# Kernel optimization log

Hardware: AMD Instinct MI355X
Metric: run time of the kernel (lower is better)

Reference implementation:

```python
import jax, jax.numpy as jnp
import numpy as np

B, T, E, H, V = 64, 21, 512, 512, 10000


def _lstm_step(x, h, c, W_ih, W_hh, b):
    # PyTorch LSTMCell gate order: i, f, g, o
    gates = x @ W_ih.T + h @ W_hh.T + b  # [B, 4H]
    i, f, g, o = jnp.split(gates, 4, axis=-1)
    i, f, o = jax.nn.sigmoid(i), jax.nn.sigmoid(f), jax.nn.sigmoid(o)
    g = jnp.tanh(g)
    c_new = f * c + i * g
    h_new = o * jnp.tanh(c_new)
    return h_new, c_new


def setup_inputs() -> dict:
    key = jax.random.key(0)
    ks = jax.random.split(key, 8)
    s_ih = 1.0 / np.sqrt(H)
    return {
        "features": jax.random.normal(ks[0], (B, E), jnp.float32),
        "caption_embedding": jax.random.normal(ks[1], (B, T, E), jnp.float32),
        "W_ih": jax.random.uniform(ks[2], (4 * H, E), jnp.float32, -s_ih, s_ih),
        "W_hh": jax.random.uniform(ks[3], (4 * H, H), jnp.float32, -s_ih, s_ih),
        "b_ih": jax.random.uniform(ks[4], (4 * H,), jnp.float32, -s_ih, s_ih),
        "b_hh": jax.random.uniform(ks[5], (4 * H,), jnp.float32, -s_ih, s_ih),
        "W_lin": jax.random.uniform(ks[6], (V, H), jnp.float32, -s_ih, s_ih),
        "b_lin": jax.random.uniform(ks[7], (V,), jnp.float32, -s_ih, s_ih),
    }


def reference(features, caption_embedding, W_ih, W_hh, b_ih, b_hh, W_lin, b_lin):
    b = b_ih + b_hh
    batch = features.shape[0]
    hidden = W_hh.shape[1]
    h0 = jnp.zeros((batch, hidden), features.dtype)
    c0 = jnp.zeros((batch, hidden), features.dtype)
    # t = 0: consume image features, no output emitted
    h, c = _lstm_step(features, h0, c0, W_ih, W_hh, b)
    # t = 1..T-1: consume caption_embedding[:, t-1], emit linear(h)
    emb_seq = jnp.swapaxes(caption_embedding[:, :-1, :], 0, 1)  # [T-1, B, E]

    def body(carry, x_t):
        h, c = carry
        h, c = _lstm_step(x_t, h, c, W_ih, W_hh, b)
        out = h @ W_lin.T + b_lin  # [B, V]
        return (h, c), out

    _, outs = jax.lax.scan(body, (h, c), emb_seq)  # [T-1, B, V]
    return jnp.swapaxes(outs, 0, 1)  # [B, T-1, V]
```

## Files before the change

### kernel.cpp

```cpp
#include <hip/hip_runtime.h>
#include <hip/hip_bf16.h>


#define NB 64
#define NT 21
#define NE 512
#define NH 512
#define NV 10000
#define G4 2048

typedef __attribute__((ext_vector_type(8))) short bf16x8;
typedef __attribute__((ext_vector_type(4))) float f32x4;
typedef __attribute__((ext_vector_type(4))) unsigned short u16x4;

#define OFF_WIH_HI   0UL
#define OFF_WIH_LO   2097152UL
#define OFF_WHH_HI   4194304UL
#define OFF_WHH_LO   6291456UL
#define OFF_WLIN_HI  8388608UL
#define OFF_XSEQ_HI  18743296UL
#define OFF_XSEQ_LO  20185088UL
#define OFF_BIAS     21626880UL
#define OFF_XIH      21635072UL
#define OFF_GHH      32645120UL
#define OFF_GHL      32776192UL
#define OFF_C        32907264UL
#define OFF_HBUF     33038336UL
#define OFF_FLG      34349056UL

__device__ inline unsigned short f2bf(float f) {
    unsigned int u = __float_as_uint(f);
    unsigned int r = u + 0x7FFFu + ((u >> 16) & 1u);
    return (unsigned short)(r >> 16);
}
__device__ inline float bf2f(unsigned short s) {
    return __uint_as_float(((unsigned int)s) << 16);
}

__device__ __forceinline__ void gl_lds16(const unsigned short* g, unsigned short* l) {
    auto gp = (const __attribute__((address_space(1))) unsigned int*)(unsigned long long)(const void*)g;
    auto lp = (__attribute__((address_space(3))) unsigned int*)(unsigned int)(unsigned long long)(void*)l;
    __builtin_amdgcn_global_load_lds(gp, lp, 16, 0, 0);
}

__device__ __forceinline__ void gl_lds16_sc(const unsigned short* g, unsigned short* l) {
    auto gp = (const __attribute__((address_space(1))) unsigned int*)(unsigned long long)(const void*)g;
    auto lp = (__attribute__((address_space(3))) unsigned int*)(unsigned int)(unsigned long long)(void*)l;
    __builtin_amdgcn_global_load_lds(gp, lp, 16, 0, 17);
}

__device__ __forceinline__ void st2_sc(unsigned short* p, unsigned short v) {
    unsigned int vv = v;
    asm volatile("global_store_short %0, %1, off sc0 sc1" :: "v"(p), "v"(vv) : "memory");
}

__global__ __launch_bounds__(256) void prep_kernel(
    const float* __restrict__ features, const float* __restrict__ cap,
    const float* __restrict__ W_ih, const float* __restrict__ W_hh,
    const float* __restrict__ b_ih, const float* __restrict__ b_hh,
    const float* __restrict__ W_lin, unsigned char* __restrict__ ws)
{
    const int idx = blockIdx.x * 256 + threadIdx.x;
    unsigned short* wih_hi = (unsigned short*)(ws + OFF_WIH_HI);
    unsigned short* wih_lo = (unsigned short*)(ws + OFF_WIH_LO);
    unsigned short* whh_hi = (unsigned short*)(ws + OFF_WHH_HI);
    unsigned short* whh_lo = (unsigned short*)(ws + OFF_WHH_LO);
    unsigned short* wlin_hi = (unsigned short*)(ws + OFF_WLIN_HI);
    unsigned short* xs_hi = (unsigned short*)(ws + OFF_XSEQ_HI);
    unsigned short* xs_lo = (unsigned short*)(ws + OFF_XSEQ_LO);
    float* bias = (float*)(ws + OFF_BIAS);

    if (idx < 262144) {
        const int i4 = idx * 4;
        float4 w = *(const float4*)(W_ih + i4);
        u16x4 hi, lo;
        hi.x = f2bf(w.x); lo.x = f2bf(w.x - bf2f(hi.x));
        hi.y = f2bf(w.y); lo.y = f2bf(w.y - bf2f(hi.y));
        hi.z = f2bf(w.z); lo.z = f2bf(w.z - bf2f(hi.z));
        hi.w = f2bf(w.w); lo.w = f2bf(w.w - bf2f(hi.w));
        *(u16x4*)(wih_hi + i4) = hi;
        *(u16x4*)(wih_lo + i4) = lo;
    } else if (idx < 524288) {
        const int i4 = (idx - 262144) * 4;
        float4 w = *(const float4*)(W_hh + i4);
        u16x4 hi, lo;
        hi.x = f2bf(w.x); lo.x = f2bf(w.x - bf2f(hi.x));
        hi.y = f2bf(w.y); lo.y = f2bf(w.y - bf2f(hi.y));
        hi.z = f2bf(w.z); lo.z = f2bf(w.z - bf2f(hi.z));
        hi.w = f2bf(w.w); lo.w = f2bf(w.w - bf2f(hi.w));
        *(u16x4*)(whh_hi + i4) = hi;
        *(u16x4*)(whh_lo + i4) = lo;
    } else if (idx < 1804288) {
        const int i4 = (idx - 524288) * 4;
        float4 w = *(const float4*)(W_lin + i4);
        u16x4 hi;
        hi.x = f2bf(w.x); hi.y = f2bf(w.y); hi.z = f2bf(w.z); hi.w = f2bf(w.w);
        *(u16x4*)(wlin_hi + i4) = hi;
    } else if (idx < 1976320) {
        const int i4 = (idx - 1804288) * 4;
        const int e = i4 & 511;
        const int b = (i4 >> 9) & 63;
        const int t = i4 >> 15;
        float4 x = (t == 0) ? *(const float4*)(features + b * NE + e)
                            : *(const float4*)(cap + b * (NT * NE) + (t - 1) * NE + e);
        u16x4 hi, lo;
        hi.x = f2bf(x.x); lo.x = f2bf(x.x - bf2f(hi.x));
        hi.y = f2bf(x.y); lo.y = f2bf(x.y - bf2f(hi.y));
        hi.z = f2bf(x.z); lo.z = f2bf(x.z - bf2f(hi.z));
        hi.w = f2bf(x.w); lo.w = f2bf(x.w - bf2f(hi.w));
        *(u16x4*)(xs_hi + i4) = hi;
        *(u16x4*)(xs_lo + i4) = lo;
    } else if (idx < 1976832) {
        const int j = (idx - 1976320) * 4;
        float4 a = *(const float4*)(b_ih + j);
        float4 b = *(const float4*)(b_hh + j);
        *(float4*)(bias + j) = make_float4(a.x + b.x, a.y + b.y, a.z + b.z, a.w + b.w);
    }
}

__global__ __launch_bounds__(256) void gemm_a_kernel(unsigned char* __restrict__ ws)
{
    __shared__ unsigned short Ah[2][4096], Al[2][4096], Bh[2][4096], Bl[2][4096];
    const int tid = threadIdx.x;
    const int lane = tid & 63, wv = tid >> 6;
    const int mf = lane & 15, kg = lane >> 4;
    const int mw = (wv >> 1) * 64, nw = (wv & 1) * 64;
    const int m0 = blockIdx.y * 128, n0 = blockIdx.x * 128;

    const unsigned short* __restrict__ xh = (const unsigned short*)(ws + OFF_XSEQ_HI);
    const unsigned short* __restrict__ xl = (const unsigned short*)(ws + OFF_XSEQ_LO);
    const unsigned short* __restrict__ wh = (const unsigned short*)(ws + OFF_WIH_HI);
    const unsigned short* __restrict__ wl = (const unsigned short*)(ws + OFF_WIH_LO);
    const float* __restrict__ bias = (const float*)(ws + OFF_BIAS);
    float* __restrict__ xih = (float*)(ws + OFF_XIH);

    f32x4 acc[4][4];
#pragma unroll
    for (int i = 0; i < 4; i++)
#pragma unroll
        for (int j = 0; j < 4; j++) acc[i][j] = (f32x4){0.f, 0.f, 0.f, 0.f};

    auto stage = [&](int buf, int k0) {
#pragma unroll
        for (int h = 0; h < 2; ++h) {
            int s = h * 256 + tid;
            int r = s >> 2, ks = (s & 3) * 8;
            gl_lds16(xh + (size_t)(m0 + r) * 512 + k0 + ks, &Ah[buf][s * 8]);
            gl_lds16(xl + (size_t)(m0 + r) * 512 + k0 + ks, &Al[buf][s * 8]);
            gl_lds16(wh + (size_t)(n0 + r) * 512 + k0 + ks, &Bh[buf][s * 8]);
            gl_lds16(wl + (size_t)(n0 + r) * 512 + k0 + ks, &Bl[buf][s * 8]);
        }
    };

    stage(0, 0);
    for (int kt = 0; kt < 16; ++kt) {
        __syncthreads();
        const int cur = kt & 1;
        if (kt < 15) stage(cur ^ 1, (kt + 1) * 32);
        bf16x8 ah[4], al[4], bh[4], bl[4];
#pragma unroll
        for (int i = 0; i < 4; i++) {
            ah[i] = *(const bf16x8*)&Ah[cur][(mw + i * 16 + mf) * 32 + kg * 8];
            al[i] = *(const bf16x8*)&Al[cur][(mw + i * 16 + mf) * 32 + kg * 8];
            bh[i] = *(const bf16x8*)&Bh[cur][(nw + i * 16 + mf) * 32 + kg * 8];
            bl[i] = *(const bf16x8*)&Bl[cur][(nw + i * 16 + mf) * 32 + kg * 8];
        }
#pragma unroll
        for (int i = 0; i < 4; i++)
#pragma unroll
            for (int j = 0; j < 4; j++) {
                acc[i][j] = __builtin_amdgcn_mfma_f32_16x16x32_bf16(ah[i], bh[j], acc[i][j], 0, 0, 0);
                acc[i][j] = __builtin_amdgcn_mfma_f32_16x16x32_bf16(ah[i], bl[j], acc[i][j], 0, 0, 0);
                acc[i][j] = __builtin_amdgcn_mfma_f32_16x16x32_bf16(al[i], bh[j], acc[i][j], 0, 0, 0);
            }
    }
#pragma unroll
    for (int i = 0; i < 4; i++)
#pragma unroll
        for (int j = 0; j < 4; j++) {
            const int col = n0 + nw + j * 16 + mf;
            const float bb = bias[col];
#pragma unroll
            for (int r = 0; r < 4; r++) {
                const int R = m0 + mw + i * 16 + kg * 4 + r;
                if (R < NT * NB) xih[(size_t)R * G4 + col] = acc[i][j][r] + bb;
            }
        }
}

__global__ __launch_bounds__(512, 2) void lstm_persistent(unsigned char* __restrict__ ws)
{
    __shared__ unsigned short Hhi[64 * 512];
    __shared__ unsigned short Hlo[64 * 512];
    __shared__ float glf[4096];
    const int tid = threadIdx.x;
    const int lane = tid & 63, wv = tid >> 6;
    const int mf = lane & 15, kg = lane >> 4;
    const int q = wv & 3;
    const int mh = wv >> 2;
    const int bc = blockIdx.x;

    unsigned short* __restrict__ ghh = (unsigned short*)(ws + OFF_GHH);
    unsigned short* __restrict__ ghl = (unsigned short*)(ws + OFF_GHL);
    const unsigned short* __restrict__ whh_hi = (const unsigned short*)(ws + OFF_WHH_HI);
    const unsigned short* __restrict__ whh_lo = (const unsigned short*)(ws + OFF_WHH_LO);
    const float* __restrict__ xih_base = (const float*)(ws + OFF_XIH);
    unsigned short* __restrict__ hbuf = (unsigned short*)(ws + OFF_HBUF);
    unsigned int* __restrict__ ctr = (unsigned int*)(ws + OFF_FLG);

    bf16x8 bh[16], blo[16];
#pragma unroll
    for (int j = 0; j < 16; ++j) {
        const size_t off = (size_t)(q * 512 + bc * 16 + mf) * 512 + j * 32 + kg * 8;
        bh[j] = *(const bf16x8*)(whh_hi + off);
        blo[j] = *(const bf16x8*)(whh_lo + off);
    }

    const int row0 = tid >> 4;
    const int row1 = row0 + 32;
    const int ci = tid & 15;
    const int c = bc * 16 + ci;
    const int jc = c >> 3;
    float creg[2] = {0.f, 0.f};

    float xp[8];
    auto load_xp = [&](int tt) {
        const float* __restrict__ xq = xih_base + (size_t)tt * NB * G4;
#pragma unroll
        for (int g = 0; g < 4; ++g) {
            xp[g]     = xq[row0 * G4 + g * 512 + c];
            xp[4 + g] = xq[row1 * G4 + g * 512 + c];
        }
    };
    load_xp(0);

    for (int t = 0; t < NT; ++t) {
        f32x4 acc[2];
        acc[0] = (f32x4){0.f, 0.f, 0.f, 0.f};
        acc[1] = (f32x4){0.f, 0.f, 0.f, 0.f};

        if (t > 0) {
            const int rd = (t + 1) & 1;
            const unsigned short* __restrict__ ghh_r = ghh + rd * (NB * NH);
            const unsigned short* __restrict__ ghl_r = ghl + rd * (NB * NH);
#pragma unroll
            for (int i = 0; i < 8; ++i) {
                const int s = i * 512 + tid;
                gl_lds16_sc(ghh_r + s * 8, &Hhi[s * 8]);
            }
#pragma unroll
            for (int i = 0; i < 8; ++i) {
                const int s = i * 512 + tid;
                gl_lds16_sc(ghl_r + s * 8, &Hlo[s * 8]);
            }
            asm volatile("s_waitcnt vmcnt(8)" ::: "memory");
            __builtin_amdgcn_s_barrier();
#pragma unroll
            for (int kt = 0; kt < 16; ++kt) {
                const int j = kt * 4 + kg;
#pragma unroll
                for (int m = 0; m < 2; ++m) {
                    const int row = mh * 32 + m * 16 + mf;
                    bf16x8 a_hi = *(const bf16x8*)&Hhi[(row * 64 + (j ^ (row & 7))) * 8];
                    acc[m] = __builtin_amdgcn_mfma_f32_16x16x32_bf16(a_hi, bh[kt], acc[m], 0, 0, 0);
                    acc[m] = __builtin_amdgcn_mfma_f32_16x16x32_bf16(a_hi, blo[kt], acc[m], 0, 0, 0);
                }
            }
            asm volatile("s_waitcnt vmcnt(0)" ::: "memory");
            __builtin_amdgcn_s_barrier();
#pragma unroll
            for (int kt = 0; kt < 16; ++kt) {
                const int j = kt * 4 + kg;
#pragma unroll
                for (int m = 0; m < 2; ++m) {
                    const int row = mh * 32 + m * 16 + mf;
                    bf16x8 a_lo = *(const bf16x8*)&Hlo[(row * 64 + (j ^ (row & 7))) * 8];
                    acc[m] = __builtin_amdgcn_mfma_f32_16x16x32_bf16(a_lo, bh[kt], acc[m], 0, 0, 0);
                }
            }
        }

#pragma unroll
        for (int m = 0; m < 2; ++m) {
            const int row = mh * 32 + m * 16 + kg * 4;
#pragma unroll
            for (int r = 0; r < 4; ++r)
                glf[(q * 64 + row + r) * 16 + mf] = acc[m][r];
        }
        __syncthreads();

        unsigned short* __restrict__ ghh_w = ghh + (t & 1) * (NB * NH);
        unsigned short* __restrict__ ghl_w = ghl + (t & 1) * (NB * NH);
#pragma unroll
        for (int cc = 0; cc < 2; ++cc) {
            const int row = cc ? row1 : row0;
            const float gi = glf[(0 * 64 + row) * 16 + ci] + xp[cc * 4 + 0];
            const float gf = glf[(1 * 64 + row) * 16 + ci] + xp[cc * 4 + 1];
            const float gg = glf[(2 * 64 + row) * 16 + ci] + xp[cc * 4 + 2];
            const float go = glf[(3 * 64 + row) * 16 + ci] + xp[cc * 4 + 3];
            const float i_ = 1.f / (1.f + __expf(-gi));
            const float f_ = 1.f / (1.f + __expf(-gf));
            const float g_ = tanhf(gg);
            const float o_ = 1.f / (1.f + __expf(-go));
            const float c_new = f_ * creg[cc] + i_ * g_;
            creg[cc] = c_new;
            const float h_new = o_ * tanhf(c_new);
            const unsigned short hi = f2bf(h_new);
            const unsigned short lo = f2bf(h_new - bf2f(hi));
            const int sw = row * 512 + ((jc ^ (row & 7)) << 3) + (c & 7);
            st2_sc(&ghh_w[sw], hi);
            st2_sc(&ghl_w[sw], lo);
            if (t >= 1)
                __builtin_nontemporal_store(hi, &hbuf[(t - 1) * (NB * NH) + row * NH + c]);
        }

        if (t < NT - 1) {
            load_xp(t + 1);
            asm volatile("s_waitcnt vmcnt(0)" ::: "memory");
            __syncthreads();
            if (tid == 0) {
                __hip_atomic_fetch_add(&ctr[t], 1u, __ATOMIC_RELAXED, __HIP_MEMORY_SCOPE_AGENT);
                while (__hip_atomic_load(&ctr[t], __ATOMIC_RELAXED, __HIP_MEMORY_SCOPE_AGENT) < 32u)
                    __builtin_amdgcn_s_sleep(1);
            }
            __syncthreads();
        }
    }
}

__global__ __launch_bounds__(256) void gemm_c_kernel(
    unsigned char* __restrict__ ws, const float* __restrict__ b_lin, float* __restrict__ out)
{
    __shared__ unsigned short As[2][4096], Bs[2][4096];
    const int tid = threadIdx.x;
    const int lane = tid & 63, wv = tid >> 6;
    const int mf = lane & 15, kg = lane >> 4;
    const int mw = (wv >> 1) * 64, nw = (wv & 1) * 64;
    const int m0 = blockIdx.y * 128, n0 = blockIdx.x * 128;

    const unsigned short* __restrict__ hb = (const unsigned short*)(ws + OFF_HBUF);
    const unsigned short* __restrict__ wlin = (const unsigned short*)(ws + OFF_WLIN_HI);

    f32x4 acc[4][4];
#pragma unroll
    for (int i = 0; i < 4; i++)
#pragma unroll
        for (int j = 0; j < 4; j++) acc[i][j] = (f32x4){0.f, 0.f, 0.f, 0.f};

    auto stage = [&](int buf, int k0) {
#pragma unroll
        for (int h = 0; h < 2; ++h) {
            int s = h * 256 + tid;
            int r = s >> 2, ks = (s & 3) * 8;
            gl_lds16(hb + (size_t)(m0 + r) * 512 + k0 + ks, &As[buf][s * 8]);
            gl_lds16(wlin + (size_t)(n0 + r) * 512 + k0 + ks, &Bs[buf][s * 8]);
        }
    };

    stage(0, 0);
    for (int kt = 0; kt < 16; ++kt) {
        __syncthreads();
        const int cur = kt & 1;
        if (kt < 15) stage(cur ^ 1, (kt + 1) * 32);
        bf16x8 af[4], bf[4];
#pragma unroll
        for (int i = 0; i < 4; i++) {
            af[i] = *(const bf16x8*)&As[cur][(mw + i * 16 + mf) * 32 + kg * 8];
            bf[i] = *(const bf16x8*)&Bs[cur][(nw + i * 16 + mf) * 32 + kg * 8];
        }
#pragma unroll
        for (int i = 0; i < 4; i++)
#pragma unroll
            for (int j = 0; j < 4; j++)
                acc[i][j] = __builtin_amdgcn_mfma_f32_16x16x32_bf16(af[i], bf[j], acc[i][j], 0, 0, 0);
    }
#pragma unroll
    for (int i = 0; i < 4; i++)
#pragma unroll
        for (int j = 0; j < 4; j++) {
            const int col = n0 + nw + j * 16 + mf;
            if (col < NV) {
                const float bl = b_lin[col];
#pragma unroll
                for (int r = 0; r < 4; r++) {
                    const int R = m0 + mw + i * 16 + kg * 4 + r;
                    const int b_ = R & 63, tt = R >> 6;
                    out[(size_t)b_ * ((NT - 1) * NV) + (size_t)tt * NV + col] = acc[i][j][r] + bl;
                }
            }
        }
}

extern "C" void kernel_launch(void* const* d_in, const int* in_sizes, int n_in,
                              void* d_out, int out_size, void* d_ws, size_t ws_size,
                              hipStream_t stream)
{
    const float* features = (const float*)d_in[0];
    const float* cap      = (const float*)d_in[1];
    const float* W_ih     = (const float*)d_in[2];
    const float* W_hh     = (const float*)d_in[3];
    const float* b_ih     = (const float*)d_in[4];
    const float* b_hh     = (const float*)d_in[5];
    const float* W_lin    = (const float*)d_in[6];
    const float* b_lin    = (const float*)d_in[7];
    float* out = (float*)d_out;
    unsigned char* ws = (unsigned char*)d_ws;

    hipMemsetAsync(ws + OFF_FLG, 0, (NT - 1) * sizeof(unsigned int), stream);

    hipLaunchKernelGGL(prep_kernel, dim3(7722), dim3(256), 0, stream,
                       features, cap, W_ih, W_hh, b_ih, b_hh, W_lin, ws);
    hipLaunchKernelGGL(gemm_a_kernel, dim3(16, 11), dim3(256), 0, stream, ws);
    hipLaunchKernelGGL(lstm_persistent, dim3(32), dim3(512), 0, stream, ws);
    hipLaunchKernelGGL(gemm_c_kernel, dim3(79, 10), dim3(256), 0, stream, ws, b_lin, out);
}
```

Before: 296.6 us.

## Fuse LSTM recurrence and output projection into one persistent kernel with per-step flags

Merges the persistent LSTM kernel and the output-projection GEMM into a single 256-block launch. Blocks 0-31 run the recurrence, and the remaining 224 blocks wait on per-block, per-timestep flags before computing each timestep's logits, so the projection overlaps the serial recurrence instead of running after it. The shared atomic counter barrier becomes padded per-block flags polled by one wavefront, and the h stores are packed into dword pairs. The risks are a deadlock if not all 256 blocks are co-resident, reuse of the old c-buffer region for the flags, and smaller GEMM tiles with less reuse.

After: 257.8 us. -13.1%, faster.

```diff
diff --git a/kernel.cpp b/kernel.cpp
--- a/kernel.cpp
+++ b/kernel.cpp
@@ -8,6 +8,7 @@
 #define NH 512
 #define NV 10000
 #define G4 2048
+#define FLGD 16
 
 typedef __attribute__((ext_vector_type(8))) short bf16x8;
 typedef __attribute__((ext_vector_type(4))) float f32x4;
@@ -49,9 +50,8 @@
     __builtin_amdgcn_global_load_lds(gp, lp, 16, 0, 17);
 }
 
-__device__ __forceinline__ void st2_sc(unsigned short* p, unsigned short v) {
-    unsigned int vv = v;
-    asm volatile("global_store_short %0, %1, off sc0 sc1" :: "v"(p), "v"(vv) : "memory");
+__device__ __forceinline__ void st4_sc(unsigned int* p, unsigned int v) {
+    asm volatile("global_store_dword %0, %1, off sc0 sc1" :: "v"(p), "v"(v) : "memory");
 }
 
 __global__ __launch_bounds__(256) void prep_kernel(
@@ -188,7 +188,8 @@
         }
 }
 
-__global__ __launch_bounds__(512, 2) void lstm_persistent(unsigned char* __restrict__ ws)
+__global__ __launch_bounds__(512, 2) void fused_persistent(
+    unsigned char* __restrict__ ws, const float* __restrict__ b_lin, float* __restrict__ out)
 {
     __shared__ unsigned short Hhi[64 * 512];
     __shared__ unsigned short Hlo[64 * 512];
@@ -196,199 +197,225 @@
     const int tid = threadIdx.x;
     const int lane = tid & 63, wv = tid >> 6;
     const int mf = lane & 15, kg = lane >> 4;
-    const int q = wv & 3;
-    const int mh = wv >> 2;
-    const int bc = blockIdx.x;
-
-    unsigned short* __restrict__ ghh = (unsigned short*)(ws + OFF_GHH);
-    unsigned short* __restrict__ ghl = (unsigned short*)(ws + OFF_GHL);
-    const unsigned short* __restrict__ whh_hi = (const unsigned short*)(ws + OFF_WHH_HI);
-    const unsigned short* __restrict__ whh_lo = (const unsigned short*)(ws + OFF_WHH_LO);
-    const float* __restrict__ xih_base = (const float*)(ws + OFF_XIH);
+
+    unsigned int* __restrict__ flg = (unsigned int*)(ws + OFF_C);
     unsigned short* __restrict__ hbuf = (unsigned short*)(ws + OFF_HBUF);
-    unsigned int* __restrict__ ctr = (unsigned int*)(ws + OFF_FLG);
-
-    bf16x8 bh[16], blo[16];
-#pragma unroll
-    for (int j = 0; j < 16; ++j) {
-        const size_t off = (size_t)(q * 512 + bc * 16 + mf) * 512 + j * 32 + kg * 8;
-        bh[j] = *(const bf16x8*)(whh_hi + off);
-        blo[j] = *(const bf16x8*)(whh_lo + off);
-    }
-
-    const int row0 = tid >> 4;
-    const int row1 = row0 + 32;
-    const int ci = tid & 15;
-    const int c = bc * 16 + ci;
-    const int jc = c >> 3;
-    float creg[2] = {0.f, 0.f};
-
-    float xp[8];
-    auto load_xp = [&](int tt) {
-        const float* __restrict__ xq = xih_base + (size_t)tt * NB * G4;
-#pragma unroll
-        for (int g = 0; g < 4; ++g) {
-            xp[g]     = xq[row0 * G4 + g * 512 + c];
-            xp[4 + g] = xq[row1 * G4 + g * 512 + c];
-        }
-    };
-    load_xp(0);
-
-    for (int t = 0; t < NT; ++t) {
-        f32x4 acc[2];
-        acc[0] = (f32x4){0.f, 0.f, 0.f, 0.f};
-        acc[1] = (f32x4){0.f, 0.f, 0.f, 0.f};
-
-        if (t > 0) {
-            const int rd = (t + 1) & 1;
-            const unsigned short* __restrict__ ghh_r = ghh + rd * (NB * NH);
-            const unsigned short* __restrict__ ghl_r = ghl + rd * (NB * NH);
-#pragma unroll
-            for (int i = 0; i < 8; ++i) {
-                const int s = i * 512 + tid;
-                gl_lds16_sc(ghh_r + s * 8, &Hhi[s * 8]);
-            }
-#pragma unroll
-            for (int i = 0; i < 8; ++i) {
-                const int s = i * 512 + tid;
-                gl_lds16_sc(ghl_r + s * 8, &Hlo[s * 8]);
-            }
-            asm volatile("s_waitcnt vmcnt(8)" ::: "memory");
-            __builtin_amdgcn_s_barrier();
-#pragma unroll
-            for (int kt = 0; kt < 16; ++kt) {
-                const int j = kt * 4 + kg;
-#pragma unroll
-                for (int m = 0; m < 2; ++m) {
-                    const int row = mh * 32 + m * 16 + mf;
-                    bf16x8 a_hi = *(const bf16x8*)&Hhi[(row * 64 + (j ^ (row & 7))) * 8];
-                    acc[m] = __builtin_amdgcn_mfma_f32_16x16x32_bf16(a_hi, bh[kt], acc[m], 0, 0, 0);
-                    acc[m] = __builtin_amdgcn_mfma_f32_16x16x32_bf16(a_hi, blo[kt], acc[m], 0, 0, 0);
-                }
-            }
-            asm volatile("s_waitcnt vmcnt(0)" ::: "memory");
-            __builtin_amdgcn_s_barrier();
-#pragma unroll
-            for (int kt = 0; kt < 16; ++kt) {
-                const int j = kt * 4 + kg;
-#pragma unroll
-                for (int m = 0; m < 2; ++m) {
-                    const int row = mh * 32 + m * 16 + mf;
-                    bf16x8 a_lo = *(const bf16x8*)&Hlo[(row * 64 + (j ^ (row & 7))) * 8];
-                    acc[m] = __builtin_amdgcn_mfma_f32_16x16x32_bf16(a_lo, bh[kt], acc[m], 0, 0, 0);
-                }
-            }
-        }
-
-#pragma unroll
-        for (int m = 0; m < 2; ++m) {
-            const int row = mh * 32 + m * 16 + kg * 4;
-#pragma unroll
-            for (int r = 0; r < 4; ++r)
-                glf[(q * 64 + row + r) * 16 + mf] = acc[m][r];
-        }
-        __syncthreads();
-
-        unsigned short* __restrict__ ghh_w = ghh + (t & 1) * (NB * NH);
-        unsigned short* __restrict__ ghl_w = ghl + (t & 1) * (NB * NH);
-#pragma unroll
-        for (int cc = 0; cc < 2; ++cc) {
-            const int row = cc ? row1 : row0;
-            const float gi = glf[(0 * 64 + row) * 16 + ci] + xp[cc * 4 + 0];
-            const float gf = glf[(1 * 64 + row) * 16 + ci] + xp[cc * 4 + 1];
-            const float gg = glf[(2 * 64 + row) * 16 + ci] + xp[cc * 4 + 2];
-            const float go = glf[(3 * 64 + row) * 16 + ci] + xp[cc * 4 + 3];
-            const float i_ = 1.f / (1.f + __expf(-gi));
-            const float f_ = 1.f / (1.f + __expf(-gf));
-            const float g_ = tanhf(gg);
-            const float o_ = 1.f / (1.f + __expf(-go));
-            const float c_new = f_ * creg[cc] + i_ * g_;
-            creg[cc] = c_new;
-            const float h_new = o_ * tanhf(c_new);
-            const unsigned short hi = f2bf(h_new);
-            const unsigned short lo = f2bf(h_new - bf2f(hi));
-            const int sw = row * 512 + ((jc ^ (row & 7)) << 3) + (c & 7);
-            st2_sc(&ghh_w[sw], hi);
-            st2_sc(&ghl_w[sw], lo);
-            if (t >= 1)
-                __builtin_nontemporal_store(hi, &hbuf[(t - 1) * (NB * NH) + row * NH + c]);
-        }
-
-        if (t < NT - 1) {
-            load_xp(t + 1);
+    const unsigned short* __restrict__ wlin = (const unsigned short*)(ws + OFF_WLIN_HI);
+
+    if (blockIdx.x < 32) {
+        const int bc = blockIdx.x;
+        const int q = wv & 3;
+        const int mh = wv >> 2;
+
+        unsigned short* __restrict__ ghh = (unsigned short*)(ws + OFF_GHH);
+        unsigned short* __restrict__ ghl = (unsigned short*)(ws + OFF_GHL);
+        const unsigned short* __restrict__ whh_hi = (const unsigned short*)(ws + OFF_WHH_HI);
+        const unsigned short* __restrict__ whh_lo = (const unsigned short*)(ws + OFF_WHH_LO);
+        const float* __restrict__ xih_base = (const float*)(ws + OFF_XIH);
+
+        bf16x8 bh[16], blo[16];
+#pragma unroll
+        for (int j = 0; j < 16; ++j) {
+            const size_t off = (size_t)(q * 512 + bc * 16 + mf) * 512 + j * 32 + kg * 8;
+            bh[j] = *(const bf16x8*)(whh_hi + off);
+            blo[j] = *(const bf16x8*)(whh_lo + off);
+        }
+
+        const int crow = tid >> 3;
+        const int cp = tid & 7;
+        const int c0 = bc * 16 + cp * 2;
+        const int jc0 = c0 >> 3;
+        float creg0 = 0.f, creg1 = 0.f;
+
+        float2 xp[4];
+        auto load_xp = [&](int tt) {
+            const float* __restrict__ xq = xih_base + (size_t)tt * NB * G4;
+#pragma unroll
+            for (int g2 = 0; g2 < 4; ++g2)
+                xp[g2] = *(const float2*)&xq[crow * G4 + g2 * 512 + c0];
+        };
+        load_xp(0);
+
+        for (int t = 0; t < NT; ++t) {
+            f32x4 acc[2];
+            acc[0] = (f32x4){0.f, 0.f, 0.f, 0.f};
+            acc[1] = (f32x4){0.f, 0.f, 0.f, 0.f};
+
+            if (t > 0) {
+                const int rd = (t + 1) & 1;
+                const unsigned short* __restrict__ ghh_r = ghh + rd * (NB * NH);
+                const unsigned short* __restrict__ ghl_r = ghl + rd * (NB * NH);
+#pragma unroll
+                for (int i = 0; i < 8; ++i) {
+                    const int s = i * 512 + tid;
+                    gl_lds16_sc(ghh_r + s * 8, &Hhi[s * 8]);
+                }
+#pragma unroll
+                for (int i = 0; i < 8; ++i) {
+                    const int s = i * 512 + tid;
+                    gl_lds16_sc(ghl_r + s * 8, &Hlo[s * 8]);
+                }
+                asm volatile("s_waitcnt vmcnt(8)" ::: "memory");
+                __builtin_amdgcn_s_barrier();
+#pragma unroll
+                for (int kt = 0; kt < 16; ++kt) {
+                    const int j = kt * 4 + kg;
+#pragma unroll
+                    for (int m = 0; m < 2; ++m) {
+                        const int row = mh * 32 + m * 16 + mf;
+                        bf16x8 a_hi = *(const bf16x8*)&Hhi[(row * 64 + (j ^ (row & 7))) * 8];
+                        acc[m] = __builtin_amdgcn_mfma_f32_16x16x32_bf16(a_hi, bh[kt], acc[m], 0, 0, 0);
+                        acc[m] = __builtin_amdgcn_mfma_f32_16x16x32_bf16(a_hi, blo[kt], acc[m], 0, 0, 0);
+                    }
+                }
+                asm volatile("s_waitcnt vmcnt(0)" ::: "memory");
+                __builtin_amdgcn_s_barrier();
+#pragma unroll
+                for (int kt = 0; kt < 16; ++kt) {
+                    const int j = kt * 4 + kg;
+#pragma unroll
+                    for (int m = 0; m < 2; ++m) {
+                        const int row = mh * 32 + m * 16 + mf;
+                        bf16x8 a_lo = *(const bf16x8*)&Hlo[(row * 64 + (j ^ (row & 7))) * 8];
+                        acc[m] = __builtin_amdgcn_mfma_f32_16x16x32_bf16(a_lo, bh[kt], acc[m], 0, 0, 0);
+                    }
+                }
+            }
+
+#pragma unroll
+            for (int m = 0; m < 2; ++m) {
+                const int row = mh * 32 + m * 16 + kg * 4;
+#pragma unroll
+                for (int r = 0; r < 4; ++r)
+                    glf[(q * 64 + row + r) * 16 + mf] = acc[m][r];
+            }
+            __syncthreads();
+
+            {
+                unsigned short* __restrict__ ghh_w = ghh + (t & 1) * (NB * NH);
+                unsigned short* __restrict__ ghl_w = ghl + (t & 1) * (NB * NH);
+                const float2 g0 = *(const float2*)&glf[(0 * 64 + crow) * 16 + cp * 2];
+                const float2 g1 = *(const float2*)&glf[(1 * 64 + crow) * 16 + cp * 2];
+                const float2 g2 = *(const float2*)&glf[(2 * 64 + crow) * 16 + cp * 2];
+                const float2 g3 = *(const float2*)&glf[(3 * 64 + crow) * 16 + cp * 2];
+                const float gi0 = g0.x + xp[0].x, gi1 = g0.y + xp[0].y;
+                const float gf0 = g1.x + xp[1].x, gf1 = g1.y + xp[1].y;
+                const float gg0 = g2.x + xp[2].x, gg1 = g2.y + xp[2].y;
+                const float go0 = g3.x + xp[3].x, go1 = g3.y + xp[3].y;
+                const float i0 = 1.f / (1.f + __expf(-gi0)), i1 = 1.f / (1.f + __expf(-gi1));
+                const float f0 = 1.f / (1.f + __expf(-gf0)), f1 = 1.f / (1.f + __expf(-gf1));
+                const float ga0 = tanhf(gg0),                ga1 = tanhf(gg1);
+                const float o0 = 1.f / (1.f + __expf(-go0)), o1 = 1.f / (1.f + __expf(-go1));
+                const float cn0 = f0 * creg0 + i0 * ga0;
+                const float cn1 = f1 * creg1 + i1 * ga1;
+                creg0 = cn0; creg1 = cn1;
+                const float h0 = o0 * tanhf(cn0);
+                const float h1 = o1 * tanhf(cn1);
+                const unsigned short hi0 = f2bf(h0), hi1 = f2bf(h1);
+                const unsigned short lo0 = f2bf(h0 - bf2f(hi0)), lo1 = f2bf(h1 - bf2f(hi1));
+                const unsigned int hpack = (unsigned int)hi0 | ((unsigned int)hi1 << 16);
+                const unsigned int lpack = (unsigned int)lo0 | ((unsigned int)lo1 << 16);
+                const int sw = crow * 512 + ((jc0 ^ (crow & 7)) << 3) + (cp & 3) * 2;
+                st4_sc((unsigned int*)&ghh_w[sw], hpack);
+                st4_sc((unsigned int*)&ghl_w[sw], lpack);
+                if (t >= 1)
+                    st4_sc((unsigned int*)&hbuf[(size_t)(t - 1) * (NB * NH) + crow * NH + c0], hpack);
+            }
+
             asm volatile("s_waitcnt vmcnt(0)" ::: "memory");
             __syncthreads();
             if (tid == 0) {
-                __hip_atomic_fetch_add(&ctr[t], 1u, __ATOMIC_RELAXED, __HIP_MEMORY_SCOPE_AGENT);
-                while (__hip_atomic_load(&ctr[t], __ATOMIC_RELAXED, __HIP_MEMORY_SCOPE_AGENT) < 32u)
-                    __builtin_amdgcn_s_sleep(1);
-            }
+                unsigned int one = 1u;
+                unsigned int* fp = flg + ((size_t)t * 32 + bc) * FLGD;
+                asm volatile("global_store_dword %0, %1, off sc0 sc1" :: "v"(fp), "v"(one) : "memory");
+            }
+            if (t < NT - 1) {
+                load_xp(t + 1);
+                if (wv == 0) {
+                    const unsigned int* fp = flg + ((size_t)t * 32 + (lane & 31)) * FLGD;
+                    while (__hip_atomic_load(fp, __ATOMIC_RELAXED, __HIP_MEMORY_SCOPE_AGENT) == 0u)
+                        __builtin_amdgcn_s_sleep(1);
+                }
+                __syncthreads();
+            }
+        }
+        asm volatile("s_waitcnt vmcnt(0)" ::: "memory");
+        return;
+    }
+
+    const int g = blockIdx.x - 32;
+    const int jt = g % 79;
+    const int rshare = g / 79;
+    const int nshare = (jt < 66) ? 3 : 2;
+    const int n0g = jt * 128;
+    const int mw2 = (wv >> 2) * 32, nw2 = (wv & 3) * 32;
+
+    unsigned short* __restrict__ AsB = Hhi;
+    unsigned short* __restrict__ BsB = Hhi + 4096;
+
+    for (int tt = rshare; tt < NT - 1; tt += nshare) {
+        if (wv == 0) {
+            const unsigned int* fp = flg + ((size_t)(tt + 1) * 32 + (lane & 31)) * FLGD;
+            while (__hip_atomic_load(fp, __ATOMIC_RELAXED, __HIP_MEMORY_SCOPE_AGENT) == 0u)
+                __builtin_amdgcn_s_sleep(2);
+        }
+        __syncthreads();
+
+        const unsigned short* __restrict__ hbA = hbuf + (size_t)tt * (NB * NH);
+        auto stageC = [&](int buf, int k0) {
+            if (tid < 256) {
+                const int s = tid;
+                const int r = s >> 2, kcol = (s & 3) * 8;
+                gl_lds16_sc(hbA + (size_t)r * 512 + k0 + kcol, &AsB[buf * 2048 + s * 8]);
+            } else {
+#pragma unroll
+                for (int h2 = 0; h2 < 2; ++h2) {
+                    const int s = h2 * 256 + (tid - 256);
+                    const int r = s >> 2, kcol = (s & 3) * 8;
+                    gl_lds16(wlin + (size_t)(n0g + r) * 512 + k0 + kcol, &BsB[buf * 4096 + s * 8]);
+                }
+            }
+        };
+
+        f32x4 acc2[2][2];
+#pragma unroll
+        for (int i = 0; i < 2; i++)
+#pragma unroll
+            for (int j = 0; j < 2; j++) acc2[i][j] = (f32x4){0.f, 0.f, 0.f, 0.f};
+
+        stageC(0, 0);
+        for (int kt = 0; kt < 16; ++kt) {
             __syncthreads();
-        }
+            const int cur = kt & 1;
+            if (kt < 15) stageC(cur ^ 1, (kt + 1) * 32);
+            bf16x8 af[2], bfv[2];
+#pragma unroll
+            for (int i = 0; i < 2; i++) {
+                af[i]  = *(const bf16x8*)&AsB[cur * 2048 + (mw2 + i * 16 + mf) * 32 + kg * 8];
+                bfv[i] = *(const bf16x8*)&BsB[cur * 4096 + (nw2 + i * 16 + mf) * 32 + kg * 8];
+            }
+#pragma unroll
+            for (int i = 0; i < 2; i++)
+#pragma unroll
+                for (int j = 0; j < 2; j++)
+                    acc2[i][j] = __builtin_amdgcn_mfma_f32_16x16x32_bf16(af[i], bfv[j], acc2[i][j], 0, 0, 0);
+        }
+#pragma unroll
+        for (int i = 0; i < 2; i++)
+#pragma unroll
+            for (int j = 0; j < 2; j++) {
+                const int col = n0g + nw2 + j * 16 + mf;
+                if (col < NV) {
+                    const float bl = b_lin[col];
+#pragma unroll
+                    for (int r = 0; r < 4; r++) {
+                        const int b_ = mw2 + i * 16 + kg * 4 + r;
+                        out[(size_t)b_ * ((NT - 1) * NV) + (size_t)tt * NV + col] = acc2[i][j][r] + bl;
+                    }
+                }
+            }
+        __syncthreads();
     }
-}
-
-__global__ __launch_bounds__(256) void gemm_c_kernel(
-    unsigned char* __restrict__ ws, const float* __restrict__ b_lin, float* __restrict__ out)
-{
-    __shared__ unsigned short As[2][4096], Bs[2][4096];
-    const int tid = threadIdx.x;
-    const int lane = tid & 63, wv = tid >> 6;
-    const int mf = lane & 15, kg = lane >> 4;
-    const int mw = (wv >> 1) * 64, nw = (wv & 1) * 64;
-    const int m0 = blockIdx.y * 128, n0 = blockIdx.x * 128;
-
-    const unsigned short* __restrict__ hb = (const unsigned short*)(ws + OFF_HBUF);
-    const unsigned short* __restrict__ wlin = (const unsigned short*)(ws + OFF_WLIN_HI);
-
-    f32x4 acc[4][4];
-#pragma unroll
-    for (int i = 0; i < 4; i++)
-#pragma unroll
-        for (int j = 0; j < 4; j++) acc[i][j] = (f32x4){0.f, 0.f, 0.f, 0.f};
-
-    auto stage = [&](int buf, int k0) {
-#pragma unroll
-        for (int h = 0; h < 2; ++h) {
-            int s = h * 256 + tid;
-            int r = s >> 2, ks = (s & 3) * 8;
-            gl_lds16(hb + (size_t)(m0 + r) * 512 + k0 + ks, &As[buf][s * 8]);
-            gl_lds16(wlin + (size_t)(n0 + r) * 512 + k0 + ks, &Bs[buf][s * 8]);
-        }
-    };
-
-    stage(0, 0);
-    for (int kt = 0; kt < 16; ++kt) {
-        __syncthreads();
-        const int cur = kt & 1;
-        if (kt < 15) stage(cur ^ 1, (kt + 1) * 32);
-        bf16x8 af[4], bf[4];
-#pragma unroll
-        for (int i = 0; i < 4; i++) {
-            af[i] = *(const bf16x8*)&As[cur][(mw + i * 16 + mf) * 32 + kg * 8];
-            bf[i] = *(const bf16x8*)&Bs[cur][(nw + i * 16 + mf) * 32 + kg * 8];
-        }
-#pragma unroll
-        for (int i = 0; i < 4; i++)
-#pragma unroll
-            for (int j = 0; j < 4; j++)
-                acc[i][j] = __builtin_amdgcn_mfma_f32_16x16x32_bf16(af[i], bf[j], acc[i][j], 0, 0, 0);
-    }
-#pragma unroll
-    for (int i = 0; i < 4; i++)
-#pragma unroll
-        for (int j = 0; j < 4; j++) {
-            const int col = n0 + nw + j * 16 + mf;
-            if (col < NV) {
-                const float bl = b_lin[col];
-#pragma unroll
-                for (int r = 0; r < 4; r++) {
-                    const int R = m0 + mw + i * 16 + kg * 4 + r;
-                    const int b_ = R & 63, tt = R >> 6;
-                    out[(size_t)b_ * ((NT - 1) * NV) + (size_t)tt * NV + col] = acc[i][j][r] + bl;
-                }
-            }
-        }
 }
 
 extern "C" void kernel_launch(void* const* d_in, const int* in_sizes, int n_in,
@@ -406,11 +433,10 @@
     float* out = (float*)d_out;
     unsigned char* ws = (unsigned char*)d_ws;
 
-    hipMemsetAsync(ws + OFF_FLG, 0, (NT - 1) * sizeof(unsigned int), stream);
+    hipMemsetAsync(ws + OFF_C, 0, (size_t)NT * 32 * FLGD * sizeof(unsigned int), stream);
 
     hipLaunchKernelGGL(prep_kernel, dim3(7722), dim3(256), 0, stream,
                        features, cap, W_ih, W_hh, b_ih, b_hh, W_lin, ws);
     hipLaunchKernelGGL(gemm_a_kernel, dim3(16, 11), dim3(256), 0, stream, ws);
-    hipLaunchKernelGGL(lstm_persistent, dim3(32), dim3(512), 0, stream, ws);
-    hipLaunchKernelGGL(gemm_c_kernel, dim3(79, 10), dim3(256), 0, stream, ws, b_lin, out);
-}
+    hipLaunchKernelGGL(fused_persistent, dim3(256), dim3(512), 0, stream, ws, b_lin, out);
+}
```
